# Optimization experiments

Measured on AMD Instinct MI355X. Metric: run time of the kernel, lower is better.

## Reference

```python
import jax, jax.numpy as jnp
import numpy as np

DMODEL, Q_HEADS, KV_HEADS, SEQ_LEN = 4096, 32, 8, 2048
HEAD_DIM = DMODEL // Q_HEADS  # 128
ROPE_BASE = 500000.0


def _rope_sin_cos(head_dim, length, base):
    # Faithful numpy port of LlamaRoPE.__init__ (llama3 frequency scaling).
    freqs = 1.0 / np.power(base, np.arange(0, head_dim, 2, dtype=np.float64) / head_dim)
    factor, low_ff, high_ff, old_ctx = 32.0, 1.0, 4.0, 8192.0
    low_wl, high_wl = old_ctx / low_ff, old_ctx / high_ff
    wavelen = 2.0 * np.pi / freqs
    inv = np.where(wavelen > low_wl, freqs / factor, freqs)
    smooth = (old_ctx / wavelen - low_ff) / (high_ff - low_ff)
    smoothed = (1.0 - smooth) * inv / factor + smooth * inv
    is_medium = (~(wavelen < high_wl)) & (~(wavelen > low_wl))
    inv = np.where(is_medium, smoothed, inv)
    angles = np.arange(length, dtype=np.float64)[:, None] * inv[None, :]  # [S, D/2]
    angles = np.concatenate([angles, angles], axis=-1)  # repeat(1,2) -> [S, D]
    return (jnp.asarray(np.sin(angles), jnp.float32),
            jnp.asarray(np.cos(angles), jnp.float32))


def _apply_rope(x, sin, cos):
    # x: [B, H, S, D]; sin/cos: [S, D]
    half = x.shape[-1] // 2
    rot = jnp.concatenate([-x[..., half:], x[..., :half]], axis=-1)
    return x * cos[None, None] + rot * sin[None, None]


def setup_inputs() -> dict:
    key = jax.random.key(0)
    kx, kq, kk, kv, ko = jax.random.split(key, 5)
    s = 0.02
    return {
        "x": jax.random.normal(kx, (2, SEQ_LEN, DMODEL), jnp.float32),
        "wq": jax.random.normal(kq, (DMODEL, DMODEL), jnp.float32) * s,
        "wk": jax.random.normal(kk, (KV_HEADS * HEAD_DIM, DMODEL), jnp.float32) * s,
        "wv": jax.random.normal(kv, (KV_HEADS * HEAD_DIM, DMODEL), jnp.float32) * s,
        "wo": jax.random.normal(ko, (DMODEL, DMODEL), jnp.float32) * s,
    }


def reference(x, wq, wk, wv, wo):
    B, S, _ = x.shape
    sin, cos = _rope_sin_cos(HEAD_DIM, SEQ_LEN, ROPE_BASE)
    # projections (nn.Linear: y = x @ W.T)
    q = (x @ wq.T).reshape(B, S, Q_HEADS, HEAD_DIM).transpose(0, 2, 1, 3)
    k = (x @ wk.T).reshape(B, S, KV_HEADS, HEAD_DIM).transpose(0, 2, 1, 3)
    v = (x @ wv.T).reshape(B, S, KV_HEADS, HEAD_DIM).transpose(0, 2, 1, 3)
    q = _apply_rope(q, sin, cos)
    k = _apply_rope(k, sin, cos)
    # GQA repeat_kv: [B, KV, S, D] -> [B, Q, S, D]
    rep = Q_HEADS // KV_HEADS
    k = jnp.repeat(k, rep, axis=1)
    v = jnp.repeat(v, rep, axis=1)
    # causal SDPA
    scale = 1.0 / jnp.sqrt(jnp.asarray(HEAD_DIM, jnp.float32))
    scores = jnp.einsum("bhqd,bhkd->bhqk", q, k) * scale
    mask = jnp.tril(jnp.ones((S, S), dtype=bool))
    scores = jnp.where(mask[None, None], scores, jnp.asarray(-jnp.inf, scores.dtype))
    attn = jax.nn.softmax(scores, axis=-1)
    out = jnp.einsum("bhqk,bhkd->bhqd", attn, v)
    out = out.transpose(0, 2, 1, 3).reshape(B, S, DMODEL)
    return out @ wo.T
```

## Files before the change

### kernel.cpp

```cpp
#include <hip/hip_runtime.h>
#include <cstdint>

#define S_LEN 2048
#define DM 4096
#define NQH 32
#define NKVH 8
#define HD 128

typedef __bf16 bf16x8 __attribute__((ext_vector_type(8)));
typedef float f32x4 __attribute__((ext_vector_type(4)));
typedef unsigned short u16;
typedef unsigned short u16x8 __attribute__((ext_vector_type(8)));
typedef unsigned int u32;

__device__ __forceinline__ float bf2f(u16 h) {
  union { u32 u; float f; } v; v.u = ((u32)h) << 16; return v.f;
}
__device__ __forceinline__ u16 f2bf(float f) {
  union { float f; u32 u; } v; v.f = f;
  u32 u = v.u;
  return (u16)((u + 0x7FFFu + ((u >> 16) & 1u)) >> 16);
}

__device__ __forceinline__ void gload16(const void* g, const void* l) {
  __builtin_amdgcn_global_load_lds(
      (const __attribute__((address_space(1))) u32*)(uintptr_t)g,
      (__attribute__((address_space(3))) u32*)(u32)(uintptr_t)l,
      16, 0, 0);
}

__device__ __forceinline__ void stage16(const float* __restrict__ g, u16* l) {
  const float4* gp = reinterpret_cast<const float4*>(g);
  float4 v0 = gp[0], v1 = gp[1], v2 = gp[2], v3 = gp[3];
  u16x8 a, b;
  a[0] = f2bf(v0.x); a[1] = f2bf(v0.y); a[2] = f2bf(v0.z); a[3] = f2bf(v0.w);
  a[4] = f2bf(v1.x); a[5] = f2bf(v1.y); a[6] = f2bf(v1.z); a[7] = f2bf(v1.w);
  b[0] = f2bf(v2.x); b[1] = f2bf(v2.y); b[2] = f2bf(v2.z); b[3] = f2bf(v2.w);
  b[4] = f2bf(v3.x); b[5] = f2bf(v3.y); b[6] = f2bf(v3.z); b[7] = f2bf(v3.w);
  *reinterpret_cast<u16x8*>(l) = a;
  *reinterpret_cast<u16x8*>(l + 8) = b;
}
__device__ __forceinline__ void stage16(const u16* __restrict__ g, u16* l) {
  *reinterpret_cast<u16x8*>(l) = *reinterpret_cast<const u16x8*>(g);
  *reinterpret_cast<u16x8*>(l + 8) = *reinterpret_cast<const u16x8*>(g + 8);
}

__device__ __forceinline__ void stc(u16* p, float v) { *p = f2bf(v); }
__device__ __forceinline__ void stc(float* p, float v) { *p = v; }

__device__ __forceinline__ void cvt8(const float* in, u16* out, size_t i8) {
  const float4* gp = reinterpret_cast<const float4*>(in) + i8 * 2;
  float4 a = gp[0], b = gp[1];
  u16x8 o;
  o[0] = f2bf(a.x); o[1] = f2bf(a.y); o[2] = f2bf(a.z); o[3] = f2bf(a.w);
  o[4] = f2bf(b.x); o[5] = f2bf(b.y); o[6] = f2bf(b.z); o[7] = f2bf(b.w);
  reinterpret_cast<u16x8*>(out)[i8] = o;
}
__global__ void cvt_all(const float* x, const float* wq, const float* wk,
                        const float* wv, const float* wo,
                        u16* xb, u16* wqkvb, u16* wob) {
  const size_t NX8 = (size_t)2 * S_LEN * DM / 8;
  const size_t NW8 = (size_t)DM * DM / 8;
  const size_t NK8 = (size_t)NKVH * HD * DM / 8;
  const size_t total = NX8 + NW8 + 2 * NK8 + NW8;
  size_t stride = (size_t)gridDim.x * blockDim.x;
  for (size_t i = (size_t)blockIdx.x * blockDim.x + threadIdx.x; i < total; i += stride) {
    if (i < NX8)                       cvt8(x,  xb,                    i);
    else if (i < NX8 + NW8)            cvt8(wq, wqkvb,                 i - NX8);
    else if (i < NX8 + NW8 + NK8)      cvt8(wk, wqkvb + NW8 * 8,       i - NX8 - NW8);
    else if (i < NX8 + NW8 + 2 * NK8)  cvt8(wv, wqkvb + (NW8 + NK8) * 8, i - NX8 - NW8 - NK8);
    else                               cvt8(wo, wob,                   i - NX8 - NW8 - 2 * NK8);
  }
}

__global__ void rope_table_kernel(float* __restrict__ sin_t, float* __restrict__ cos_t) {
  int idx = blockIdx.x * blockDim.x + threadIdx.x;
  if (idx >= S_LEN * 64) return;
  int s = idx >> 6, i = idx & 63;
  const double PI = 3.14159265358979323846;
  double freq = pow(500000.0, -((double)i) / 64.0);
  double wavelen = 2.0 * PI / freq;
  double inv = (wavelen > 8192.0) ? freq / 32.0 : freq;
  if (!(wavelen < 2048.0) && !(wavelen > 8192.0)) {
    double smooth = (8192.0 / wavelen - 1.0) / 3.0;
    inv = (1.0 - smooth) * (freq / 32.0) + smooth * freq;
  }
  double ang = (double)s * inv;
  sin_t[idx] = (float)sin(ang);
  cos_t[idx] = (float)cos(ang);
}

__global__ void rope_apply(u16* __restrict__ X, const float* __restrict__ sin_t,
                           const float* __restrict__ cos_t, float scale, int nrows) {
  int idx = blockIdx.x * blockDim.x + threadIdx.x;
  if (idx >= nrows * 64) return;
  int row = idx >> 6, i = idx & 63;
  int s = row & (S_LEN - 1);
  size_t base = (size_t)row * HD;
  float lo = bf2f(X[base + i]);
  float hi = bf2f(X[base + i + 64]);
  float sn = sin_t[s * 64 + i];
  float cs = cos_t[s * 64 + i];
  X[base + i] = f2bf((lo * cs - hi * sn) * scale);
  X[base + i + 64] = f2bf((hi * cs + lo * sn) * scale);
}

template <int MODE, typename TC>
__global__ __launch_bounds__(256, 4)
void gemm16(const u16* __restrict__ A, const u16* __restrict__ B,
            TC* __restrict__ C, int M, int N, int K, int H) {
  __shared__ u16 sA[128 * 64];
  __shared__ u16 sB[128 * 64];
  const int tid = threadIdx.x;
  const int lane = tid & 63;
  const int wv = tid >> 6;
  const int wr = wv >> 1, wc = wv & 1;
  const int bm = blockIdx.y * 128;
  const int bn = blockIdx.x * 128;
  const int fr = lane & 15, fq = lane >> 4;
  const int srow_base = wv * 8 + (lane >> 3);
  const int sgran = (((lane & 7) ^ ((lane >> 3) & 7))) * 8;
  const int rxor = fr & 7;

  f32x4 zero4 = {0.f, 0.f, 0.f, 0.f};
  f32x4 acc[4][4];
#pragma unroll
  for (int i = 0; i < 4; ++i)
#pragma unroll
    for (int j = 0; j < 4; ++j) acc[i][j] = zero4;

  for (int k0 = 0; k0 < K; k0 += 64) {
    __syncthreads();
#pragma unroll
    for (int g = 0; g < 4; ++g) {
      int row = g * 32 + srow_base;
      gload16(A + (size_t)(bm + row) * K + k0 + sgran, sA + g * 2048 + wv * 512);
      gload16(B + (size_t)(bn + row) * K + k0 + sgran, sB + g * 2048 + wv * 512);
    }
    __syncthreads();
#pragma unroll
    for (int kk = 0; kk < 2; ++kk) {
      bf16x8 af[4], bg[4];
      const int gofs = ((kk * 4 + fq) ^ rxor) * 8;
#pragma unroll
      for (int i = 0; i < 4; ++i) {
        af[i] = *(const bf16x8*)(sA + (wr * 64 + i * 16 + fr) * 64 + gofs);
        bg[i] = *(const bf16x8*)(sB + (wc * 64 + i * 16 + fr) * 64 + gofs);
      }
#pragma unroll
      for (int i = 0; i < 4; ++i)
#pragma unroll
        for (int j = 0; j < 4; ++j)
          acc[i][j] = __builtin_amdgcn_mfma_f32_16x16x32_bf16(af[i], bg[j], acc[i][j], 0, 0, 0);
    }
  }

#pragma unroll
  for (int i = 0; i < 4; ++i)
#pragma unroll
    for (int j = 0; j < 4; ++j)
#pragma unroll
      for (int r = 0; r < 4; ++r) {
        int m = bm + wr * 64 + i * 16 + fq * 4 + r;
        int n = bn + wc * 64 + j * 16 + fr;
        stc(C + (size_t)m * N + n, acc[i][j][r]);
      }
}

__global__ __launch_bounds__(256, 4)
void gemm_qkv(const u16* __restrict__ A, const u16* __restrict__ B,
              u16* __restrict__ Cq, u16* __restrict__ Ck, u16* __restrict__ Cv,
              int K) {
  __shared__ u16 sA[128 * 64];
  __shared__ u16 sB[128 * 64];
  const int tid = threadIdx.x;
  const int lane = tid & 63;
  const int wv = tid >> 6;
  const int wr = wv >> 1, wc = wv & 1;
  const int bm = blockIdx.y * 128;
  const int bn = blockIdx.x * 128;
  const int fr = lane & 15, fq = lane >> 4;
  const int srow_base = wv * 8 + (lane >> 3);
  const int sgran = (((lane & 7) ^ ((lane >> 3) & 7))) * 8;
  const int rxor = fr & 7;

  f32x4 zero4 = {0.f, 0.f, 0.f, 0.f};
  f32x4 acc[4][4];
#pragma unroll
  for (int i = 0; i < 4; ++i)
#pragma unroll
    for (int j = 0; j < 4; ++j) acc[i][j] = zero4;

  for (int k0 = 0; k0 < K; k0 += 64) {
    __syncthreads();
#pragma unroll
    for (int g = 0; g < 4; ++g) {
      int row = g * 32 + srow_base;
      gload16(A + (size_t)(bm + row) * K + k0 + sgran, sA + g * 2048 + wv * 512);
      gload16(B + (size_t)(bn + row) * K + k0 + sgran, sB + g * 2048 + wv * 512);
    }
    __syncthreads();
#pragma unroll
    for (int kk = 0; kk < 2; ++kk) {
      bf16x8 af[4], bg[4];
      const int gofs = ((kk * 4 + fq) ^ rxor) * 8;
#pragma unroll
      for (int i = 0; i < 4; ++i) {
        af[i] = *(const bf16x8*)(sA + (wr * 64 + i * 16 + fr) * 64 + gofs);
        bg[i] = *(const bf16x8*)(sB + (wc * 64 + i * 16 + fr) * 64 + gofs);
      }
#pragma unroll
      for (int i = 0; i < 4; ++i)
#pragma unroll
        for (int j = 0; j < 4; ++j)
          acc[i][j] = __builtin_amdgcn_mfma_f32_16x16x32_bf16(af[i], bg[j], acc[i][j], 0, 0, 0);
    }
  }

#pragma unroll
  for (int i = 0; i < 4; ++i)
#pragma unroll
    for (int j = 0; j < 4; ++j)
#pragma unroll
      for (int r = 0; r < 4; ++r) {
        int m = bm + wr * 64 + i * 16 + fq * 4 + r;
        int n = bn + wc * 64 + j * 16 + fr;
        int b = m >> 11, s = m & 2047;
        u16 hval = f2bf(acc[i][j][r]);
        if (n < 4096) {
          int hh = n >> 7, d = n & 127;
          Cq[(((size_t)(b * NQH + hh)) * S_LEN + s) * HD + d] = hval;
        } else if (n < 5120) {
          int nn = n - 4096;
          int hh = nn >> 7, d = nn & 127;
          Ck[(((size_t)(b * NKVH + hh)) * S_LEN + s) * HD + d] = hval;
        } else {
          int nn = n - 5120;
          int hh = nn >> 7, d = nn & 127;
          Cv[(((size_t)(b * NKVH + hh)) * HD + d) * S_LEN + s] = hval;
        }
      }
}

template <int MODE, typename TA, typename TB, typename TC>
__global__ __launch_bounds__(256, 2)
void gemm_bt(const TA* __restrict__ A, const TB* __restrict__ B,
             TC* __restrict__ C, int M, int N, int K, int H) {
  __shared__ u16 sA[128 * 32];
  __shared__ u16 sB[128 * 32];
  const int tid = threadIdx.x;
  const int lane = tid & 63;
  const int wv = tid >> 6;
  const int wr = wv >> 1, wc = wv & 1;
  const int bm = blockIdx.y * 128;
  const int bn = blockIdx.x * 128;
  const int fr = lane & 15, fq = lane >> 4;
  const int srow = tid >> 1;
  const int shalf = (tid & 1) * 16;

  f32x4 zero4 = {0.f, 0.f, 0.f, 0.f};
  f32x4 acc[4][4];
#pragma unroll
  for (int i = 0; i < 4; ++i)
#pragma unroll
    for (int j = 0; j < 4; ++j) acc[i][j] = zero4;

  for (int k0 = 0; k0 < K; k0 += 32) {
    __syncthreads();
    stage16(A + (size_t)(bm + srow) * K + k0 + shalf, sA + srow * 32 + shalf);
    stage16(B + (size_t)(bn + srow) * K + k0 + shalf, sB + srow * 32 + shalf);
    __syncthreads();
    bf16x8 af[4], bg[4];
#pragma unroll
    for (int i = 0; i < 4; ++i) {
      af[i] = *(const bf16x8*)(sA + (wr * 64 + i * 16 + fr) * 32 + fq * 8);
      bg[i] = *(const bf16x8*)(sB + (wc * 64 + i * 16 + fr) * 32 + fq * 8);
    }
#pragma unroll
    for (int i = 0; i < 4; ++i)
#pragma unroll
      for (int j = 0; j < 4; ++j)
        acc[i][j] = __builtin_amdgcn_mfma_f32_16x16x32_bf16(af[i], bg[j], acc[i][j], 0, 0, 0);
  }

#pragma unroll
  for (int i = 0; i < 4; ++i)
#pragma unroll
    for (int j = 0; j < 4; ++j)
#pragma unroll
      for (int r = 0; r < 4; ++r) {
        int m = bm + wr * 64 + i * 16 + fq * 4 + r;
        int n = bn + wc * 64 + j * 16 + fr;
        float v = acc[i][j][r];
        if (MODE == 0) {
          stc(C + (size_t)m * N + n, v);
        } else if (MODE == 1) {
          int b = m >> 11, s = m & 2047, hh = n >> 7, d = n & 127;
          stc(C + (((size_t)(b * H + hh)) * S_LEN + s) * HD + d, v);
        } else {
          int b = m >> 11, s = m & 2047, hh = n >> 7, d = n & 127;
          stc(C + (((size_t)(b * H + hh)) * HD + d) * S_LEN + s, v);
        }
      }
}

__global__ __launch_bounds__(256, 2)
void attn_kernel(const u16* __restrict__ Q, const u16* __restrict__ K,
                 const u16* __restrict__ V, u16* __restrict__ O,
                 const float* __restrict__ sin_t, const float* __restrict__ cos_t,
                 float scale) {
  __shared__ u16 sK[2][64 * 128];
  __shared__ u16 sV[2][128 * 64];
  __shared__ u16 sP[4][16 * 64];

  const int tid = threadIdx.x, lane = tid & 63, wv = tid >> 6;
  const int fr = lane & 15, fq = lane >> 4;
  const int bx = blockIdx.x;
  const int bh = blockIdx.y;
  const int b = bh >> 5, h = bh & 31;
  const int hkv = h >> 2;
  const u16* Qb = Q + (size_t)bh * S_LEN * HD;
  const u16* Kb = K + (size_t)(b * NKVH + hkv) * S_LEN * HD;
  const u16* Vb = V + (size_t)(b * NKVH + hkv) * HD * S_LEN;

  const int krow_l = lane >> 4, ke_l = lane & 15;
  const int vrow_l = lane >> 3, ve_l = lane & 7;

  for (int half = 0; half < 2; ++half) {
    const int q0 = (half == 0 ? (15 - bx) : bx) * 128;

    u16x8 qfu[2][4];
#pragma unroll
    for (int u = 0; u < 2; ++u) {
      int qrow = q0 + wv * 32 + u * 16 + fr;
      const u16* qp = Qb + (size_t)qrow * HD;
      u16x8 raw[4];
#pragma unroll
      for (int ks = 0; ks < 4; ++ks)
        raw[ks] = *(const u16x8*)(qp + ks * 32 + fq * 8);
#pragma unroll
      for (int p = 0; p < 2; ++p) {
        const float* cb = cos_t + (size_t)qrow * 64 + p * 32 + fq * 8;
        const float* sb = sin_t + (size_t)qrow * 64 + p * 32 + fq * 8;
        float4 c0 = ((const float4*)cb)[0], c1 = ((const float4*)cb)[1];
        float4 s0 = ((const float4*)sb)[0], s1 = ((const float4*)sb)[1];
        float cs[8] = {c0.x, c0.y, c0.z, c0.w, c1.x, c1.y, c1.z, c1.w};
        float sn[8] = {s0.x, s0.y, s0.z, s0.w, s1.x, s1.y, s1.z, s1.w};
#pragma unroll
        for (int j = 0; j < 8; ++j) {
          float lo = bf2f(raw[p][j]);
          float hi = bf2f(raw[p + 2][j]);
          qfu[u][p][j]     = f2bf((lo * cs[j] - hi * sn[j]) * scale);
          qfu[u][p + 2][j] = f2bf((hi * cs[j] + lo * sn[j]) * scale);
        }
      }
    }
    const bf16x8* qf0 = (const bf16x8*)&qfu[0][0];
    const bf16x8* qf1 = (const bf16x8*)&qfu[1][0];

    f32x4 zero4 = {0.f, 0.f, 0.f, 0.f};
    f32x4 o[2][8];
    float m[2][4], l[2][4];
#pragma unroll
    for (int u = 0; u < 2; ++u) {
#pragma unroll
      for (int dt = 0; dt < 8; ++dt) o[u][dt] = zero4;
#pragma unroll
      for (int r = 0; r < 4; ++r) { m[u][r] = -3.0e38f; l[u][r] = 0.f; }
    }

    const int ntiles = (q0 >> 6) + 2;

    auto STAGE = [&](int buf, int t) {
      const int s0k = t * 64;
#pragma unroll
      for (int j = 0; j < 4; ++j) {
        int c = j * 4 + wv;
        {
          int row = c * 4 + krow_l;
          int e = (ke_l ^ (row & 7)) * 8;
          gload16(Kb + (size_t)(s0k + row) * HD + e, sK[buf] + c * 512);
        }
        {
          int row = c * 8 + vrow_l;
          int e = (ve_l ^ (row & 7)) * 8;
          gload16(Vb + (size_t)row * S_LEN + s0k + e, sV[buf] + c * 512);
        }
      }
    };

    STAGE(0, 0);
    __syncthreads();
    int cur = 0;

    for (int t = 0; t < ntiles; ++t) {
      const int s0 = t * 64;
      if (t + 1 < ntiles) STAGE(cur ^ 1, t + 1);

      const u16* sKc = sK[cur];
      const u16* sVc = sV[cur];

      f32x4 sc[2][4];
#pragma unroll
      for (int u = 0; u < 2; ++u)
#pragma unroll
        for (int j = 0; j < 4; ++j) sc[u][j] = zero4;
      __builtin_amdgcn_s_setprio(1);
#pragma unroll
      for (int j = 0; j < 4; ++j) {
#pragma unroll
        for (int ks = 0; ks < 4; ++ks) {
          int row = j * 16 + fr;
          int e = (ks * 32 + fq * 8) ^ ((row & 7) << 3);
          bf16x8 kf = *(const bf16x8*)(sKc + row * 128 + e);
          sc[0][j] = __builtin_amdgcn_mfma_f32_16x16x32_bf16(qf0[ks], kf, sc[0][j], 0, 0, 0);
          sc[1][j] = __builtin_amdgcn_mfma_f32_16x16x32_bf16(qf1[ks], kf, sc[1][j], 0, 0, 0);
        }
      }
      __builtin_amdgcn_s_setprio(0);

      if (t >= ntiles - 2) {
#pragma unroll
        for (int u = 0; u < 2; ++u)
#pragma unroll
          for (int j = 0; j < 4; ++j)
#pragma unroll
            for (int r = 0; r < 4; ++r) {
              int kvp = s0 + j * 16 + fr;
              int qp = q0 + wv * 32 + u * 16 + fq * 4 + r;
              if (kvp > qp) sc[u][j][r] = -3.0e38f;
            }
      }

      bf16x8 pa[2][2];
#pragma unroll
      for (int u = 0; u < 2; ++u) {
        float al[4];
        bool resc = false;
#pragma unroll
        for (int r = 0; r < 4; ++r) {
          float v = fmaxf(fmaxf(sc[u][0][r], sc[u][1][r]), fmaxf(sc[u][2][r], sc[u][3][r]));
          v = fmaxf(v, __shfl_xor(v, 1, 64));
          v = fmaxf(v, __shfl_xor(v, 2, 64));
          v = fmaxf(v, __shfl_xor(v, 4, 64));
          v = fmaxf(v, __shfl_xor(v, 8, 64));
          if (v > m[u][r] + 8.f) {
            al[r] = __expf(m[u][r] - v);
            m[u][r] = v;
            resc = true;
          } else {
            al[r] = 1.f;
          }
        }
#pragma unroll
        for (int r = 0; r < 4; ++r) {
          float rs = 0.f;
          int prow = fq * 4 + r;
#pragma unroll
          for (int j = 0; j < 4; ++j) {
            float pv = __expf(sc[u][j][r] - m[u][r]);
            rs += pv;
            int e = (j * 16 + fr) ^ ((prow & 7) << 3);
            sP[wv][prow * 64 + e] = f2bf(pv);
          }
          l[u][r] = l[u][r] * al[r] + rs;
        }
        if (resc) {
#pragma unroll
          for (int r = 0; r < 4; ++r)
#pragma unroll
            for (int dt = 0; dt < 8; ++dt) o[u][dt][r] *= al[r];
        }
#pragma unroll
        for (int ks = 0; ks < 2; ++ks) {
          int e = (ks * 32 + fq * 8) ^ ((fr & 7) << 3);
          pa[u][ks] = *(const bf16x8*)(&sP[wv][fr * 64 + e]);
        }
      }

      __builtin_amdgcn_s_setprio(1);
#pragma unroll
      for (int dt = 0; dt < 8; ++dt) {
#pragma unroll
        for (int ks = 0; ks < 2; ++ks) {
          int row = dt * 16 + fr;
          int e = (ks * 32 + fq * 8) ^ ((row & 7) << 3);
          bf16x8 vf = *(const bf16x8*)(sVc + row * 64 + e);
#pragma unroll
          for (int u = 0; u < 2; ++u)
            o[u][dt] = __builtin_amdgcn_mfma_f32_16x16x32_bf16(pa[u][ks], vf, o[u][dt], 0, 0, 0);
        }
      }
      __builtin_amdgcn_s_setprio(0);

      __syncthreads();
      cur ^= 1;
    }

#pragma unroll
    for (int u = 0; u < 2; ++u)
#pragma unroll
      for (int r = 0; r < 4; ++r) {
        float lt = l[u][r];
        lt += __shfl_xor(lt, 1, 64);
        lt += __shfl_xor(lt, 2, 64);
        lt += __shfl_xor(lt, 4, 64);
        lt += __shfl_xor(lt, 8, 64);
        int qp = q0 + wv * 32 + u * 16 + fq * 4 + r;
        float inv_l = 1.0f / lt;
        size_t base = ((size_t)b * S_LEN + qp) * DM + h * HD;
#pragma unroll
        for (int dt = 0; dt < 8; ++dt)
          O[base + dt * 16 + fr] = f2bf(o[u][dt][r] * inv_l);
      }
  }
}

extern "C" void kernel_launch(void* const* d_in, const int* in_sizes, int n_in,
                              void* d_out, int out_size, void* d_ws, size_t ws_size,
                              hipStream_t stream) {
  const float* x  = (const float*)d_in[0];
  const float* wq = (const float*)d_in[1];
  const float* wk = (const float*)d_in[2];
  const float* wv = (const float*)d_in[3];
  const float* wo = (const float*)d_in[4];

  char* ws = (char*)d_ws;
  size_t off = 0;
  auto alloc = [&](size_t bytes) {
    void* p = ws + off;
    off += (bytes + 255) & ~(size_t)255;
    return p;
  };

  const size_t nx  = (size_t)2 * S_LEN * DM;
  const size_t nwq = (size_t)DM * DM;
  const size_t nwk = (size_t)(NKVH * HD) * DM;

  const float scale = 0.08838834764831845f;
  const int nrk = 2 * NKVH * S_LEN;
  dim3 blk(256);

  if (ws_size >= ((size_t)180 << 20)) {
    u16* xb    = (u16*)alloc(nx * 2);
    u16* wqkvb = (u16*)alloc((nwq + 2 * nwk) * 2);
    u16* wob   = (u16*)alloc(nwq * 2);
    u16* qb    = (u16*)alloc(nx * 2);
    u16* kb    = (u16*)alloc(nwk * 2);
    u16* vtb   = (u16*)alloc(nwk * 2);
    float* sin_t = (float*)alloc((size_t)S_LEN * 64 * 4);
    float* cos_t = (float*)alloc((size_t)S_LEN * 64 * 4);
    u16* aob = xb;

    cvt_all<<<2048, 256, 0, stream>>>(x, wq, wk, wv, wo, xb, wqkvb, wob);
    rope_table_kernel<<<(S_LEN * 64 + 255) / 256, 256, 0, stream>>>(sin_t, cos_t);

    gemm_qkv<<<dim3(48, 32), blk, 0, stream>>>(xb, wqkvb, qb, kb, vtb, DM);

    rope_apply<<<((size_t)nrk * 64 + 255) / 256, 256, 0, stream>>>(kb, sin_t, cos_t, 1.0f, nrk);

    attn_kernel<<<dim3(8, 64), blk, 0, stream>>>(qb, kb, vtb, aob, sin_t, cos_t, scale);

    gemm16<0, float><<<dim3(32, 32), blk, 0, stream>>>(aob, wob, (float*)d_out, 4096, DM, DM, 0);
  } else {
    u16* qb  = (u16*)alloc(nx * 2);
    u16* kb  = (u16*)alloc(nwk * 2);
    u16* vtb = (u16*)alloc(nwk * 2);
    u16* aob = (u16*)alloc(nx * 2);
    float* sin_t = (float*)alloc((size_t)S_LEN * 64 * 4);
    float* cos_t = (float*)alloc((size_t)S_LEN * 64 * 4);

    rope_table_kernel<<<(S_LEN * 64 + 255) / 256, 256, 0, stream>>>(sin_t, cos_t);

    gemm_bt<1, float, float, u16><<<dim3(32, 32), blk, 0, stream>>>(x, wq, qb, 4096, DM, DM, NQH);
    gemm_bt<1, float, float, u16><<<dim3(8, 32), blk, 0, stream>>>(x, wk, kb, 4096, 1024, DM, NKVH);
    gemm_bt<2, float, float, u16><<<dim3(8, 32), blk, 0, stream>>>(x, wv, vtb, 4096, 1024, DM, NKVH);

    rope_apply<<<((size_t)nrk * 64 + 255) / 256, 256, 0, stream>>>(kb, sin_t, cos_t, 1.0f, nrk);

    attn_kernel<<<dim3(8, 64), blk, 0, stream>>>(qb, kb, vtb, aob, sin_t, cos_t, scale);

    gemm_bt<0, u16, float, float><<<dim3(32, 32), blk, 0, stream>>>(aob, wo, (float*)d_out, 4096, DM, DM, 0);
  }
}
```

Before: 573.0 us.

## Triple-buffer GEMM shared-memory tiles with async prefetch and a single barrier

Both GEMM kernels move from a single 64-wide K tile with two barriers per step to a three-stage ring of 32-wide K tiles. The next tile is prefetched while the current one is consumed, using manual vmcnt waits and one s_barrier per step. The LDS swizzle is reworked for the narrower tile. The goal is to hide global-to-LDS load latency behind MFMA work, at the cost of occupancy (launch bounds drop from 4 to 3) and more loop iterations. A three-stage ring with only one barrier per step is a delicate hazard pattern.

Result: slower. 629.3 us (+9.8%).

```diff
diff --git a/kernel.cpp b/kernel.cpp
--- a/kernel.cpp
+++ b/kernel.cpp
@@ -106,11 +106,11 @@
 }
 
 template <int MODE, typename TC>
-__global__ __launch_bounds__(256, 4)
+__global__ __launch_bounds__(256, 3)
 void gemm16(const u16* __restrict__ A, const u16* __restrict__ B,
             TC* __restrict__ C, int M, int N, int K, int H) {
-  __shared__ u16 sA[128 * 64];
-  __shared__ u16 sB[128 * 64];
+  __shared__ u16 sA[3][128 * 32];
+  __shared__ u16 sB[3][128 * 32];
   const int tid = threadIdx.x;
   const int lane = tid & 63;
   const int wv = tid >> 6;
@@ -118,9 +118,9 @@
   const int bm = blockIdx.y * 128;
   const int bn = blockIdx.x * 128;
   const int fr = lane & 15, fq = lane >> 4;
-  const int srow_base = wv * 8 + (lane >> 3);
-  const int sgran = (((lane & 7) ^ ((lane >> 3) & 7))) * 8;
-  const int rxor = fr & 7;
+  const int srow = lane >> 2;
+  const int scol = (((lane & 3) ^ ((lane >> 3) & 3)) * 8);
+  const int rsw = (fr >> 1) & 3;
 
   f32x4 zero4 = {0.f, 0.f, 0.f, 0.f};
   f32x4 acc[4][4];
@@ -129,30 +129,46 @@
 #pragma unroll
     for (int j = 0; j < 4; ++j) acc[i][j] = zero4;
 
-  for (int k0 = 0; k0 < K; k0 += 64) {
-    __syncthreads();
-#pragma unroll
-    for (int g = 0; g < 4; ++g) {
-      int row = g * 32 + srow_base;
-      gload16(A + (size_t)(bm + row) * K + k0 + sgran, sA + g * 2048 + wv * 512);
-      gload16(B + (size_t)(bn + row) * K + k0 + sgran, sB + g * 2048 + wv * 512);
-    }
-    __syncthreads();
-#pragma unroll
-    for (int kk = 0; kk < 2; ++kk) {
-      bf16x8 af[4], bg[4];
-      const int gofs = ((kk * 4 + fq) ^ rxor) * 8;
-#pragma unroll
-      for (int i = 0; i < 4; ++i) {
-        af[i] = *(const bf16x8*)(sA + (wr * 64 + i * 16 + fr) * 64 + gofs);
-        bg[i] = *(const bf16x8*)(sB + (wc * 64 + i * 16 + fr) * 64 + gofs);
-      }
-#pragma unroll
-      for (int i = 0; i < 4; ++i)
-#pragma unroll
-        for (int j = 0; j < 4; ++j)
-          acc[i][j] = __builtin_amdgcn_mfma_f32_16x16x32_bf16(af[i], bg[j], acc[i][j], 0, 0, 0);
-    }
+  auto STAGE = [&](int buf, int k0) {
+#pragma unroll
+    for (int j = 0; j < 2; ++j) {
+      int c = j * 4 + wv;
+      int row = c * 16 + srow;
+      gload16(A + (size_t)(bm + row) * K + k0 + scol, sA[buf] + c * 512);
+      gload16(B + (size_t)(bn + row) * K + k0 + scol, sB[buf] + c * 512);
+    }
+  };
+
+  const int NT = K / 32;
+  STAGE(0, 0);
+  int buf = 0;
+  for (int t = 0; t < NT; ++t) {
+    if (t + 1 < NT) {
+      int nb = buf + 1; if (nb == 3) nb = 0;
+      STAGE(nb, (t + 1) * 32);
+      __builtin_amdgcn_sched_barrier(0);
+      asm volatile("s_waitcnt vmcnt(4)" ::: "memory");
+    } else {
+      asm volatile("s_waitcnt vmcnt(0)" ::: "memory");
+    }
+    __builtin_amdgcn_s_barrier();
+    __builtin_amdgcn_sched_barrier(0);
+
+    const u16* pA = sA[buf];
+    const u16* pB = sB[buf];
+    bf16x8 af[4], bg[4];
+#pragma unroll
+    for (int i = 0; i < 4; ++i) {
+      af[i] = *(const bf16x8*)(pA + (wr * 64 + i * 16 + fr) * 32 + (fq ^ rsw) * 8);
+      bg[i] = *(const bf16x8*)(pB + (wc * 64 + i * 16 + fr) * 32 + (fq ^ rsw) * 8);
+    }
+#pragma unroll
+    for (int i = 0; i < 4; ++i)
+#pragma unroll
+      for (int j = 0; j < 4; ++j)
+        acc[i][j] = __builtin_amdgcn_mfma_f32_16x16x32_bf16(af[i], bg[j], acc[i][j], 0, 0, 0);
+
+    buf = buf + 1; if (buf == 3) buf = 0;
   }
 
 #pragma unroll
@@ -167,12 +183,12 @@
       }
 }
 
-__global__ __launch_bounds__(256, 4)
+__global__ __launch_bounds__(256, 3)
 void gemm_qkv(const u16* __restrict__ A, const u16* __restrict__ B,
               u16* __restrict__ Cq, u16* __restrict__ Ck, u16* __restrict__ Cv,
               int K) {
-  __shared__ u16 sA[128 * 64];
-  __shared__ u16 sB[128 * 64];
+  __shared__ u16 sA[3][128 * 32];
+  __shared__ u16 sB[3][128 * 32];
   const int tid = threadIdx.x;
   const int lane = tid & 63;
   const int wv = tid >> 6;
@@ -180,9 +196,9 @@
   const int bm = blockIdx.y * 128;
   const int bn = blockIdx.x * 128;
   const int fr = lane & 15, fq = lane >> 4;
-  const int srow_base = wv * 8 + (lane >> 3);
-  const int sgran = (((lane & 7) ^ ((lane >> 3) & 7))) * 8;
-  const int rxor = fr & 7;
+  const int srow = lane >> 2;
+  const int scol = (((lane & 3) ^ ((lane >> 3) & 3)) * 8);
+  const int rsw = (fr >> 1) & 3;
 
   f32x4 zero4 = {0.f, 0.f, 0.f, 0.f};
   f32x4 acc[4][4];
@@ -191,30 +207,46 @@
 #pragma unroll
     for (int j = 0; j < 4; ++j) acc[i][j] = zero4;
 
-  for (int k0 = 0; k0 < K; k0 += 64) {
-    __syncthreads();
-#pragma unroll
-    for (int g = 0; g < 4; ++g) {
-      int row = g * 32 + srow_base;
-      gload16(A + (size_t)(bm + row) * K + k0 + sgran, sA + g * 2048 + wv * 512);
-      gload16(B + (size_t)(bn + row) * K + k0 + sgran, sB + g * 2048 + wv * 512);
-    }
-    __syncthreads();
-#pragma unroll
-    for (int kk = 0; kk < 2; ++kk) {
-      bf16x8 af[4], bg[4];
-      const int gofs = ((kk * 4 + fq) ^ rxor) * 8;
-#pragma unroll
-      for (int i = 0; i < 4; ++i) {
-        af[i] = *(const bf16x8*)(sA + (wr * 64 + i * 16 + fr) * 64 + gofs);
-        bg[i] = *(const bf16x8*)(sB + (wc * 64 + i * 16 + fr) * 64 + gofs);
-      }
-#pragma unroll
-      for (int i = 0; i < 4; ++i)
-#pragma unroll
-        for (int j = 0; j < 4; ++j)
-          acc[i][j] = __builtin_amdgcn_mfma_f32_16x16x32_bf16(af[i], bg[j], acc[i][j], 0, 0, 0);
-    }
+  auto STAGE = [&](int buf, int k0) {
+#pragma unroll
+    for (int j = 0; j < 2; ++j) {
+      int c = j * 4 + wv;
+      int row = c * 16 + srow;
+      gload16(A + (size_t)(bm + row) * K + k0 + scol, sA[buf] + c * 512);
+      gload16(B + (size_t)(bn + row) * K + k0 + scol, sB[buf] + c * 512);
+    }
+  };
+
+  const int NT = K / 32;
+  STAGE(0, 0);
+  int buf = 0;
+  for (int t = 0; t < NT; ++t) {
+    if (t + 1 < NT) {
+      int nb = buf + 1; if (nb == 3) nb = 0;
+      STAGE(nb, (t + 1) * 32);
+      __builtin_amdgcn_sched_barrier(0);
+      asm volatile("s_waitcnt vmcnt(4)" ::: "memory");
+    } else {
+      asm volatile("s_waitcnt vmcnt(0)" ::: "memory");
+    }
+    __builtin_amdgcn_s_barrier();
+    __builtin_amdgcn_sched_barrier(0);
+
+    const u16* pA = sA[buf];
+    const u16* pB = sB[buf];
+    bf16x8 af[4], bg[4];
+#pragma unroll
+    for (int i = 0; i < 4; ++i) {
+      af[i] = *(const bf16x8*)(pA + (wr * 64 + i * 16 + fr) * 32 + (fq ^ rsw) * 8);
+      bg[i] = *(const bf16x8*)(pB + (wc * 64 + i * 16 + fr) * 32 + (fq ^ rsw) * 8);
+    }
+#pragma unroll
+    for (int i = 0; i < 4; ++i)
+#pragma unroll
+      for (int j = 0; j < 4; ++j)
+        acc[i][j] = __builtin_amdgcn_mfma_f32_16x16x32_bf16(af[i], bg[j], acc[i][j], 0, 0, 0);
+
+    buf = buf + 1; if (buf == 3) buf = 0;
   }
 
 #pragma unroll
```
